# Kernel tuning notes

Measured on AMD Instinct MI355X. Metric: run time of the kernel, lower is better.

Reference implementation:

```python
import jax, jax.numpy as jnp
import numpy as np

IN_FEATURES = 2048
OUT_FEATURES = 2048
ORDER = 8
BATCH = 8192


def setup_inputs() -> dict:
    key = jax.random.key(0)
    k1, k2, k3, k4 = jax.random.split(key, 4)
    x = jax.random.normal(k1, (BATCH, IN_FEATURES), dtype=jnp.float32)
    v = jax.random.normal(k2, (ORDER, max(IN_FEATURES, OUT_FEATURES)), dtype=jnp.float32)
    d = jax.random.normal(k3, (min(IN_FEATURES, OUT_FEATURES),), dtype=jnp.float32)
    bias = jax.random.normal(k4, (OUT_FEATURES,), dtype=jnp.float32) * 0.01
    return {"x": x, "v": v, "d": d, "bias": bias}


def reference(x, v, d, bias):
    # Normalize each reflection vector (row-wise L2 norm), as in the torch module.
    n = v.shape[1]  # max_feature = 2048
    vn = v / jnp.linalg.norm(v, axis=1, keepdims=True)
    # Householder matrices H_i = I - 2 v_i v_i^T, shape [order, n, n]
    H = jnp.eye(n, dtype=x.dtype)[None, :, :] - 2.0 * jnp.einsum('ab,ac->abc', vn, vn)
    # Chain multiply u = H_0 @ H_1 @ ... @ H_{order-1} (order is a small static constant)
    u = H[0]
    for i in range(1, H.shape[0]):
        u = u @ H[i]
    # out_features <= in_features branch: W = u @ (eye(in, out) @ diag(d))
    # eye(in, out) @ diag(d) places d on the leading diagonal of an [in, out] matrix,
    # so W = u[:, :out] * d (column scaling) -- same math, no dense diag matmul.
    W = u[:, :OUT_FEATURES] * d[None, :]
    y = x @ W + bias[None, :]
    return y
```

## Files before the change

kernel.cpp:

```cpp
#include <hip/hip_runtime.h>

#define N_FEAT 2048
#define ORDER 8
#define BATCH 8192
#define BLOCK 256
#define ROWS 4

typedef float v4f __attribute__((ext_vector_type(4)));

__device__ __forceinline__ float dot4(v4f a, v4f b) {
    return a.x * b.x + a.y * b.y + a.z * b.z + a.w * b.w;
}

__global__ __launch_bounds__(BLOCK) void prep_kernel(
    const float* __restrict__ v, float* __restrict__ vn) {
    const int tid = threadIdx.x;
    const int lane = tid & 63, wid = tid >> 6;

    v4f a0[ORDER], a1[ORDER];
    #pragma unroll
    for (int i = 0; i < ORDER; ++i) {
        a0[i] = *(const v4f*)(v + (size_t)i * N_FEAT + tid * 4);
        a1[i] = *(const v4f*)(v + (size_t)i * N_FEAT + 1024 + tid * 4);
    }
    float ss[ORDER];
    #pragma unroll
    for (int i = 0; i < ORDER; ++i)
        ss[i] = dot4(a0[i], a0[i]) + dot4(a1[i], a1[i]);
    #pragma unroll
    for (int o = 32; o > 0; o >>= 1)
        #pragma unroll
        for (int i = 0; i < ORDER; ++i) ss[i] += __shfl_down(ss[i], o, 64);

    __shared__ float red[4][ORDER];
    if (lane == 0) {
        #pragma unroll
        for (int i = 0; i < ORDER; ++i) red[wid][i] = ss[i];
    }
    __syncthreads();
    #pragma unroll
    for (int i = 0; i < ORDER; ++i) {
        const float inv = 1.0f / sqrtf(red[0][i] + red[1][i] + red[2][i] + red[3][i]);
        *(v4f*)(vn + (size_t)i * N_FEAT + tid * 4) = a0[i] * inv;
        *(v4f*)(vn + (size_t)i * N_FEAT + 1024 + tid * 4) = a1[i] * inv;
    }
}

__global__ __launch_bounds__(BLOCK) void orth_apply_kernel(
    const float* __restrict__ x, const float* __restrict__ vn,
    const float* __restrict__ d, const float* __restrict__ bias,
    float* __restrict__ y) {
    const int tid = threadIdx.x;
    const int lane = tid & 63, wid = tid >> 6;
    const size_t base = (size_t)blockIdx.x * ROWS * N_FEAT;
    const int c0 = tid * 4;
    const int c1 = 1024 + tid * 4;

    v4f z0[ROWS], z1[ROWS];
    #pragma unroll
    for (int r = 0; r < ROWS; ++r) {
        z0[r] = *(const v4f*)(x + base + (size_t)r * N_FEAT + c0);
        z1[r] = *(const v4f*)(x + base + (size_t)r * N_FEAT + c1);
    }

    __shared__ float red[2][4][ROWS];

    #pragma unroll
    for (int i = 0; i < ORDER; ++i) {
        const float* vr = vn + (size_t)i * N_FEAT;
        const v4f a0 = *(const v4f*)(vr + c0);
        const v4f a1 = *(const v4f*)(vr + c1);

        float p[ROWS];
        #pragma unroll
        for (int r = 0; r < ROWS; ++r)
            p[r] = dot4(z0[r], a0) + dot4(z1[r], a1);
        #pragma unroll
        for (int o = 32; o > 0; o >>= 1)
            #pragma unroll
            for (int r = 0; r < ROWS; ++r) p[r] += __shfl_down(p[r], o, 64);

        const int buf = i & 1;
        if (lane == 0) {
            #pragma unroll
            for (int r = 0; r < ROWS; ++r) red[buf][wid][r] = p[r];
        }
        __syncthreads();

        #pragma unroll
        for (int r = 0; r < ROWS; ++r) {
            const float s = -2.0f * (red[buf][0][r] + red[buf][1][r] +
                                     red[buf][2][r] + red[buf][3][r]);
            z0[r] += s * a0;
            z1[r] += s * a1;
        }
    }

    const v4f d0 = *(const v4f*)(d + c0);
    const v4f d1 = *(const v4f*)(d + c1);
    const v4f b0 = *(const v4f*)(bias + c0);
    const v4f b1 = *(const v4f*)(bias + c1);

    #pragma unroll
    for (int r = 0; r < ROWS; ++r) {
        v4f o0 = z0[r] * d0 + b0;
        v4f o1 = z1[r] * d1 + b1;
        __builtin_nontemporal_store(o0, (v4f*)(y + base + (size_t)r * N_FEAT + c0));
        __builtin_nontemporal_store(o1, (v4f*)(y + base + (size_t)r * N_FEAT + c1));
    }
}

extern "C" void kernel_launch(void* const* d_in, const int* in_sizes, int n_in,
                              void* d_out, int out_size, void* d_ws, size_t ws_size,
                              hipStream_t stream) {
    const float* x    = (const float*)d_in[0];
    const float* v    = (const float*)d_in[1];
    const float* d    = (const float*)d_in[2];
    const float* bias = (const float*)d_in[3];
    float* y  = (float*)d_out;
    float* vn = (float*)d_ws;

    prep_kernel<<<1, BLOCK, 0, stream>>>(v, vn);
    orth_apply_kernel<<<BATCH / ROWS, BLOCK, 0, stream>>>(x, vn, d, bias, y);
}
```

Baseline: 126.8 us.

## Assign rows per wavefront to drop block-level barriers in Householder apply

Each 64-lane wavefront now owns two full rows, and each lane holds eight 4-float chunks per row. The per-reflection dot product is reduced entirely with xor shuffles inside the wavefront, so the shared-memory reduction and __syncthreads per reflection are removed. The x loads also switch to nontemporal. In exchange, each lane holds more live registers and reloads more vn data per row, since each wave reads the whole vector rows.

```diff
diff --git a/kernel.cpp b/kernel.cpp
--- a/kernel.cpp
+++ b/kernel.cpp
@@ -4,7 +4,8 @@
 #define ORDER 8
 #define BATCH 8192
 #define BLOCK 256
-#define ROWS 4
+#define RPW 2
+#define CHUNKS 8
 
 typedef float v4f __attribute__((ext_vector_type(4)));
 
@@ -50,63 +51,63 @@
     const float* __restrict__ x, const float* __restrict__ vn,
     const float* __restrict__ d, const float* __restrict__ bias,
     float* __restrict__ y) {
-    const int tid = threadIdx.x;
-    const int lane = tid & 63, wid = tid >> 6;
-    const size_t base = (size_t)blockIdx.x * ROWS * N_FEAT;
-    const int c0 = tid * 4;
-    const int c1 = 1024 + tid * 4;
+    const int lane = threadIdx.x & 63;
+    const int wid  = threadIdx.x >> 6;
+    const int wg   = blockIdx.x * (BLOCK / 64) + wid;
+    const size_t row0 = (size_t)wg * RPW;
+    const int coff = lane * 4;
 
-    v4f z0[ROWS], z1[ROWS];
+    v4f z[RPW][CHUNKS];
     #pragma unroll
-    for (int r = 0; r < ROWS; ++r) {
-        z0[r] = *(const v4f*)(x + base + (size_t)r * N_FEAT + c0);
-        z1[r] = *(const v4f*)(x + base + (size_t)r * N_FEAT + c1);
-    }
-
-    __shared__ float red[2][4][ROWS];
+    for (int r = 0; r < RPW; ++r)
+        #pragma unroll
+        for (int k = 0; k < CHUNKS; ++k)
+            z[r][k] = __builtin_nontemporal_load(
+                (const v4f*)(x + (row0 + r) * N_FEAT + k * 256 + coff));
 
     #pragma unroll
     for (int i = 0; i < ORDER; ++i) {
         const float* vr = vn + (size_t)i * N_FEAT;
-        const v4f a0 = *(const v4f*)(vr + c0);
-        const v4f a1 = *(const v4f*)(vr + c1);
+        v4f a[CHUNKS];
+        #pragma unroll
+        for (int k = 0; k < CHUNKS; ++k)
+            a[k] = *(const v4f*)(vr + k * 256 + coff);
 
-        float p[ROWS];
+        float p[RPW];
         #pragma unroll
-        for (int r = 0; r < ROWS; ++r)
-            p[r] = dot4(z0[r], a0) + dot4(z1[r], a1);
+        for (int r = 0; r < RPW; ++r) {
+            const float t0 = dot4(z[r][0], a[0]) + dot4(z[r][1], a[1]);
+            const float t1 = dot4(z[r][2], a[2]) + dot4(z[r][3], a[3]);
+            const float t2 = dot4(z[r][4], a[4]) + dot4(z[r][5], a[5]);
+            const float t3 = dot4(z[r][6], a[6]) + dot4(z[r][7], a[7]);
+            p[r] = (t0 + t1) + (t2 + t3);
+        }
+
         #pragma unroll
         for (int o = 32; o > 0; o >>= 1)
             #pragma unroll
-            for (int r = 0; r < ROWS; ++r) p[r] += __shfl_down(p[r], o, 64);
-
-        const int buf = i & 1;
-        if (lane == 0) {
-            #pragma unroll
-            for (int r = 0; r < ROWS; ++r) red[buf][wid][r] = p[r];
-        }
-        __syncthreads();
+            for (int r = 0; r < RPW; ++r)
+                p[r] += __shfl_xor(p[r], o, 64);
 
         #pragma unroll
-        for (int r = 0; r < ROWS; ++r) {
-            const float s = -2.0f * (red[buf][0][r] + red[buf][1][r] +
-                                     red[buf][2][r] + red[buf][3][r]);
-            z0[r] += s * a0;
-            z1[r] += s * a1;
+        for (int r = 0; r < RPW; ++r) {
+            const float s = -2.0f * p[r];
+            #pragma unroll
+            for (int k = 0; k < CHUNKS; ++k)
+                z[r][k] += s * a[k];
         }
     }
 
-    const v4f d0 = *(const v4f*)(d + c0);
-    const v4f d1 = *(const v4f*)(d + c1);
-    const v4f b0 = *(const v4f*)(bias + c0);
-    const v4f b1 = *(const v4f*)(bias + c1);
-
     #pragma unroll
-    for (int r = 0; r < ROWS; ++r) {
-        v4f o0 = z0[r] * d0 + b0;
-        v4f o1 = z1[r] * d1 + b1;
-        __builtin_nontemporal_store(o0, (v4f*)(y + base + (size_t)r * N_FEAT + c0));
-        __builtin_nontemporal_store(o1, (v4f*)(y + base + (size_t)r * N_FEAT + c1));
+    for (int k = 0; k < CHUNKS; ++k) {
+        const v4f dk = *(const v4f*)(d + k * 256 + coff);
+        const v4f bk = *(const v4f*)(bias + k * 256 + coff);
+        #pragma unroll
+        for (int r = 0; r < RPW; ++r) {
+            v4f o = z[r][k] * dk + bk;
+            __builtin_nontemporal_store(
+                o, (v4f*)(y + (row0 + r) * N_FEAT + k * 256 + coff));
+        }
     }
 }
 
@@ -121,5 +122,6 @@
     float* vn = (float*)d_ws;
 
     prep_kernel<<<1, BLOCK, 0, stream>>>(v, vn);
-    orth_apply_kernel<<<BATCH / ROWS, BLOCK, 0, stream>>>(x, vn, d, bias, y);
+    orth_apply_kernel<<<BATCH / (RPW * (BLOCK / 64)), BLOCK, 0, stream>>>(
+        x, vn, d, bias, y);
 }
```

After: 133.2 us. +5.0%, slower.

## Apply Householder chain via compact-WY T matrix with a single reduction

Applied to the files above, without the earlier changes.

The prep kernel now also computes the Gram matrix of the normalized reflection vectors and builds the upper-triangular compact-WY factor T, so the product of reflections becomes I - V T V^T. The apply kernel computes all eight projections at once, does one cross-wave reduction and one block barrier instead of eight, mixes the projections through T, and then applies the rank-8 update. This removes the serialized per-reflection shuffle-reduce-sync chain. In exchange it uses more registers and a tiny serial T computation on one thread, and the input loads of x are switched to nontemporal loads.

```diff
diff --git a/kernel.cpp b/kernel.cpp
--- a/kernel.cpp
+++ b/kernel.cpp
@@ -5,6 +5,7 @@
 #define BATCH 8192
 #define BLOCK 256
 #define ROWS 4
+#define NPAIR 28
 
 typedef float v4f __attribute__((ext_vector_type(4)));
 
@@ -13,7 +14,8 @@
 }
 
 __global__ __launch_bounds__(BLOCK) void prep_kernel(
-    const float* __restrict__ v, float* __restrict__ vn) {
+    const float* __restrict__ v, float* __restrict__ vn,
+    float* __restrict__ Tm) {
     const int tid = threadIdx.x;
     const int lane = tid & 63, wid = tid >> 6;
 
@@ -33,6 +35,7 @@
         for (int i = 0; i < ORDER; ++i) ss[i] += __shfl_down(ss[i], o, 64);
 
     __shared__ float red[4][ORDER];
+    __shared__ float gred[4][NPAIR];
     if (lane == 0) {
         #pragma unroll
         for (int i = 0; i < ORDER; ++i) red[wid][i] = ss[i];
@@ -41,15 +44,71 @@
     #pragma unroll
     for (int i = 0; i < ORDER; ++i) {
         const float inv = 1.0f / sqrtf(red[0][i] + red[1][i] + red[2][i] + red[3][i]);
-        *(v4f*)(vn + (size_t)i * N_FEAT + tid * 4) = a0[i] * inv;
-        *(v4f*)(vn + (size_t)i * N_FEAT + 1024 + tid * 4) = a1[i] * inv;
+        a0[i] *= inv; a1[i] *= inv;
+        *(v4f*)(vn + (size_t)i * N_FEAT + tid * 4) = a0[i];
+        *(v4f*)(vn + (size_t)i * N_FEAT + 1024 + tid * 4) = a1[i];
+    }
+
+    float gp[NPAIR];
+    {
+        int idx = 0;
+        #pragma unroll
+        for (int j = 0; j < ORDER; ++j)
+            #pragma unroll
+            for (int k = j + 1; k < ORDER; ++k)
+                gp[idx++] = dot4(a0[j], a0[k]) + dot4(a1[j], a1[k]);
+    }
+    #pragma unroll
+    for (int o = 32; o > 0; o >>= 1)
+        #pragma unroll
+        for (int q = 0; q < NPAIR; ++q) gp[q] += __shfl_down(gp[q], o, 64);
+    if (lane == 0) {
+        #pragma unroll
+        for (int q = 0; q < NPAIR; ++q) gred[wid][q] = gp[q];
+    }
+    __syncthreads();
+
+    if (tid == 0) {
+        float G[ORDER][ORDER];
+        {
+            int idx = 0;
+            #pragma unroll
+            for (int j = 0; j < ORDER; ++j)
+                #pragma unroll
+                for (int k = j + 1; k < ORDER; ++k) {
+                    G[j][k] = gred[0][idx] + gred[1][idx] + gred[2][idx] + gred[3][idx];
+                    ++idx;
+                }
+        }
+        float T[ORDER][ORDER];
+        #pragma unroll
+        for (int j = 0; j < ORDER; ++j)
+            #pragma unroll
+            for (int k = 0; k < ORDER; ++k) T[j][k] = 0.0f;
+        T[0][0] = 2.0f;
+        #pragma unroll
+        for (int k = 1; k < ORDER; ++k) {
+            #pragma unroll
+            for (int j = 0; j < k; ++j) {
+                float s = 0.0f;
+                #pragma unroll
+                for (int m = j; m < k; ++m) s += T[j][m] * G[m][k];
+                T[j][k] = -2.0f * s;
+            }
+            T[k][k] = 2.0f;
+        }
+        #pragma unroll
+        for (int j = 0; j < ORDER; ++j)
+            #pragma unroll
+            for (int k = 0; k < ORDER; ++k)
+                Tm[j * ORDER + k] = T[j][k];
     }
 }
 
 __global__ __launch_bounds__(BLOCK) void orth_apply_kernel(
     const float* __restrict__ x, const float* __restrict__ vn,
-    const float* __restrict__ d, const float* __restrict__ bias,
-    float* __restrict__ y) {
+    const float* __restrict__ Tm, const float* __restrict__ d,
+    const float* __restrict__ bias, float* __restrict__ y) {
     const int tid = threadIdx.x;
     const int lane = tid & 63, wid = tid >> 6;
     const size_t base = (size_t)blockIdx.x * ROWS * N_FEAT;
@@ -59,40 +118,68 @@
     v4f z0[ROWS], z1[ROWS];
     #pragma unroll
     for (int r = 0; r < ROWS; ++r) {
-        z0[r] = *(const v4f*)(x + base + (size_t)r * N_FEAT + c0);
-        z1[r] = *(const v4f*)(x + base + (size_t)r * N_FEAT + c1);
-    }
-
-    __shared__ float red[2][4][ROWS];
-
-    #pragma unroll
-    for (int i = 0; i < ORDER; ++i) {
-        const float* vr = vn + (size_t)i * N_FEAT;
-        const v4f a0 = *(const v4f*)(vr + c0);
-        const v4f a1 = *(const v4f*)(vr + c1);
-
-        float p[ROWS];
+        z0[r] = __builtin_nontemporal_load((const v4f*)(x + base + (size_t)r * N_FEAT + c0));
+        z1[r] = __builtin_nontemporal_load((const v4f*)(x + base + (size_t)r * N_FEAT + c1));
+    }
+
+    float p[ROWS][ORDER];
+    #pragma unroll
+    for (int i = 0; i < ORDER; ++i) {
+        const v4f a0 = *(const v4f*)(vn + (size_t)i * N_FEAT + c0);
+        const v4f a1 = *(const v4f*)(vn + (size_t)i * N_FEAT + c1);
         #pragma unroll
         for (int r = 0; r < ROWS; ++r)
-            p[r] = dot4(z0[r], a0) + dot4(z1[r], a1);
-        #pragma unroll
-        for (int o = 32; o > 0; o >>= 1)
-            #pragma unroll
-            for (int r = 0; r < ROWS; ++r) p[r] += __shfl_down(p[r], o, 64);
-
-        const int buf = i & 1;
-        if (lane == 0) {
-            #pragma unroll
-            for (int r = 0; r < ROWS; ++r) red[buf][wid][r] = p[r];
-        }
-        __syncthreads();
-
+            p[r][i] = dot4(z0[r], a0) + dot4(z1[r], a1);
+    }
+
+    #pragma unroll
+    for (int o = 32; o > 0; o >>= 1)
+        #pragma unroll
+        for (int r = 0; r < ROWS; ++r)
+            #pragma unroll
+            for (int i = 0; i < ORDER; ++i)
+                p[r][i] += __shfl_down(p[r][i], o, 64);
+
+    __shared__ float red[4][ROWS][ORDER];
+    if (lane == 0) {
+        #pragma unroll
+        for (int r = 0; r < ROWS; ++r)
+            #pragma unroll
+            for (int i = 0; i < ORDER; ++i) red[wid][r][i] = p[r][i];
+    }
+    __syncthreads();
+
+    #pragma unroll
+    for (int r = 0; r < ROWS; ++r)
+        #pragma unroll
+        for (int i = 0; i < ORDER; ++i)
+            p[r][i] = red[0][r][i] + red[1][r][i] + red[2][r][i] + red[3][r][i];
+
+    float c[ROWS][ORDER];
+    #pragma unroll
+    for (int i = 0; i < ORDER; ++i)
         #pragma unroll
         for (int r = 0; r < ROWS; ++r) {
-            const float s = -2.0f * (red[buf][0][r] + red[buf][1][r] +
-                                     red[buf][2][r] + red[buf][3][r]);
-            z0[r] += s * a0;
-            z1[r] += s * a1;
+            float s = 0.0f;
+            #pragma unroll
+            for (int j = 0; j <= i; ++j) s += p[r][j] * Tm[j * ORDER + i];
+            c[r][i] = s;
+        }
+
+    const float* vnr;
+    {
+        unsigned long long pv = (unsigned long long)vn;
+        asm volatile("" : "+s"(pv));
+        vnr = (const float*)pv;
+    }
+    #pragma unroll
+    for (int i = 0; i < ORDER; ++i) {
+        const v4f a0 = *(const v4f*)(vnr + (size_t)i * N_FEAT + c0);
+        const v4f a1 = *(const v4f*)(vnr + (size_t)i * N_FEAT + c1);
+        #pragma unroll
+        for (int r = 0; r < ROWS; ++r) {
+            z0[r] -= c[r][i] * a0;
+            z1[r] -= c[r][i] * a1;
         }
     }
 
@@ -100,7 +187,6 @@
     const v4f d1 = *(const v4f*)(d + c1);
     const v4f b0 = *(const v4f*)(bias + c0);
     const v4f b1 = *(const v4f*)(bias + c1);
-
     #pragma unroll
     for (int r = 0; r < ROWS; ++r) {
         v4f o0 = z0[r] * d0 + b0;
@@ -119,7 +205,8 @@
     const float* bias = (const float*)d_in[3];
     float* y  = (float*)d_out;
     float* vn = (float*)d_ws;
-
-    prep_kernel<<<1, BLOCK, 0, stream>>>(v, vn);
-    orth_apply_kernel<<<BATCH / ROWS, BLOCK, 0, stream>>>(x, vn, d, bias, y);
-}
+    float* Tm = vn + ORDER * N_FEAT;
+
+    prep_kernel<<<1, BLOCK, 0, stream>>>(v, vn, Tm);
+    orth_apply_kernel<<<BATCH / ROWS, BLOCK, 0, stream>>>(x, vn, Tm, d, bias, y);
+}
```

Result: slower. 142.0 us (+12.0%).
